# Kernel optimization log

Hardware: AMD Instinct MI355X
Metric: run time of the kernel (lower is better)

Reference implementation:

```python
import jax, jax.numpy as jnp
import numpy as np

N = 1 << 20          # number of sample points (rays x samples)
ENC = 32             # hash-grid encoded dim (16 levels x 2 features)
HID = 64
GEO = 15


def setup_inputs() -> dict:
    key = jax.random.key(0)
    ks = jax.random.split(key, 16)
    sc = lambda fan_in: 1.0 / np.sqrt(fan_in)
    return {
        "x": jax.random.normal(ks[0], (N, ENC), jnp.float32),
        "d": jax.random.normal(ks[1], (N, ENC), jnp.float32),
        # sigma net: ENC -> 64 -> 64 -> 1+GEO, bias-free, stored [in, out]
        "Ws0": jax.random.normal(ks[2], (ENC, HID), jnp.float32) * sc(ENC),
        "Ws1": jax.random.normal(ks[3], (HID, HID), jnp.float32) * sc(HID),
        "Ws2": jax.random.normal(ks[4], (HID, 1 + GEO), jnp.float32) * sc(HID),
        # color net: ENC+GEO -> 64 -> 64 -> 64 -> 3, bias-free
        "Wc0": jax.random.normal(ks[5], (ENC + GEO, HID), jnp.float32) * sc(ENC + GEO),
        "Wc1": jax.random.normal(ks[6], (HID, HID), jnp.float32) * sc(HID),
        "Wc2": jax.random.normal(ks[7], (HID, HID), jnp.float32) * sc(HID),
        "Wc3": jax.random.normal(ks[8], (HID, 3), jnp.float32) * sc(HID),
    }


def reference(x, d, Ws0, Ws1, Ws2, Wc0, Wc1, Wc2, Wc3):
    # sigma network: ReLU after EVERY layer (including the last, as in source)
    h = x
    for W in (Ws0, Ws1, Ws2):
        h = jax.nn.relu(h @ W)
    sigma = h[..., 0]            # [N]
    geo_feat = h[..., 1:]        # [N, GEO]

    # color network: ReLU on all but last layer, then sigmoid
    h = jnp.concatenate([d, geo_feat], axis=-1)   # [N, ENC+GEO]
    color_ws = (Wc0, Wc1, Wc2, Wc3)
    for i, W in enumerate(color_ws):
        h = h @ W
        if i != len(color_ws) - 1:
            h = jax.nn.relu(h)
    color = jax.nn.sigmoid(h)    # [N, 3]
    return color, sigma
```

## Files before the change

kernel.cpp:

```cpp
#include <hip/hip_runtime.h>
#include <hip/hip_bf16.h>

typedef short s8v __attribute__((ext_vector_type(8)));
typedef float f4v __attribute__((ext_vector_type(4)));

#define MFMA_BF16 __builtin_amdgcn_mfma_f32_16x16x32_bf16

constexpr int OFF_W0T  = 0;
constexpr int OFF_W1T  = 2560;
constexpr int OFF_W2T  = 7168;
constexpr int OFF_WC0T = 8320;
constexpr int OFF_WC1T = 12928;
constexpr int OFF_WC2T = 17536;
constexpr int OFF_WC3T = 22144;
constexpr int SMEM_EL  = 23296;

static __device__ __forceinline__ short bf2s(__hip_bfloat16 h) {
    union { __hip_bfloat16 b; short s; } u; u.b = h; return u.s;
}

__global__ __launch_bounds__(512, 2)
void rf_fused(const void* __restrict__ xv,
              const void* __restrict__ dv,
              const void* __restrict__ Ws0,
              const void* __restrict__ Ws1,
              const void* __restrict__ Ws2,
              const void* __restrict__ Wc0,
              const void* __restrict__ Wc1,
              const void* __restrict__ Wc2,
              const void* __restrict__ Wc3,
              void* __restrict__ outp,
              int npts)
{
    __shared__ __align__(16) short smem[SMEM_EL];
    __shared__ int cls_cnt;
    const int t = threadIdx.x;

    if (t == 0) cls_cnt = 0;
    __syncthreads();
    {
        unsigned short w = ((const unsigned short*)xv)[2 * t];
        int e = (w >> 7) & 0xFF;
        if (e >= 110 && e <= 140) atomicAdd(&cls_cnt, 1);
    }
    __syncthreads();
    const bool isbf = (cls_cnt >= 256);

    auto ldw = [&](const void* p, int idx) -> short {
        if (isbf) return ((const short*)p)[idx];
        return bf2s(__float2bfloat16(((const float*)p)[idx]));
    };

    for (int i = t; i < 2048; i += 512) { int k = i >> 6, n = i & 63; smem[OFF_W0T  + n*40 + k] = ldw(Ws0, i); }
    for (int i = t; i < 4096; i += 512) { int k = i >> 6, n = i & 63; smem[OFF_W1T  + n*72 + k] = ldw(Ws1, i); }
    for (int i = t; i < 1024; i += 512) { int k = i >> 4, n = i & 15; smem[OFF_W2T  + n*72 + k] = ldw(Ws2, i); }
    for (int i = t; i < 4096; i += 512) {
        int n = i >> 6, k = i & 63;
        short v = 0;
        if (k < 32)                 v = ldw(Wc0, k*64 + n);
        else if (k >= 33 && k < 48) v = ldw(Wc0, (k-1)*64 + n);
        smem[OFF_WC0T + n*72 + k] = v;
    }
    for (int i = t; i < 4096; i += 512) { int k = i >> 6, n = i & 63; smem[OFF_WC1T + n*72 + k] = ldw(Wc1, i); }
    for (int i = t; i < 4096; i += 512) { int k = i >> 6, n = i & 63; smem[OFF_WC2T + n*72 + k] = ldw(Wc2, i); }
    for (int i = t; i < 1024; i += 512) { int n = i >> 6, k = i & 63; smem[OFF_WC3T + n*72 + k] = (n < 3) ? ldw(Wc3, k*3 + n) : (short)0; }
    __syncthreads();

    const int lane = t & 63;
    const int wv   = t >> 6;
    const int m16  = lane & 15;
    const int q    = lane >> 4;

    const f4v zf = {0.f, 0.f, 0.f, 0.f};

    s8v w0f[4], w1f[4][2], wc0f[4][2], wc1f[4][2], wc2f[4][2], w2f[2], wc3f[2];
    #pragma unroll
    for (int kt = 0; kt < 4; kt++) {
        w0f[kt] = *(const s8v*)(smem + OFF_W0T + (kt*16 + m16)*40 + q*8);
        #pragma unroll
        for (int h = 0; h < 2; h++) {
            w1f[kt][h]  = *(const s8v*)(smem + OFF_W1T  + (kt*16 + m16)*72 + h*32 + q*8);
            wc0f[kt][h] = *(const s8v*)(smem + OFF_WC0T + (kt*16 + m16)*72 + h*32 + q*8);
            wc1f[kt][h] = *(const s8v*)(smem + OFF_WC1T + (kt*16 + m16)*72 + h*32 + q*8);
            wc2f[kt][h] = *(const s8v*)(smem + OFF_WC2T + (kt*16 + m16)*72 + h*32 + q*8);
        }
    }
    #pragma unroll
    for (int h = 0; h < 2; h++) {
        w2f[h]  = *(const s8v*)(smem + OFF_W2T  + m16*72 + h*32 + q*8);
        wc3f[h] = *(const s8v*)(smem + OFF_WC3T + m16*72 + h*32 + q*8);
    }

    auto loadRow8f = [&](const void* p, int eoff) -> s8v {
        const float* f = (const float*)p + eoff;
        f4v f0 = *(const f4v*)f;
        f4v f1 = *(const f4v*)(f + 4);
        s8v r;
        #pragma unroll
        for (int j = 0; j < 4; j++) {
            r[j]     = bf2s(__float2bfloat16(f0[j]));
            r[j + 4] = bf2s(__float2bfloat16(f1[j]));
        }
        return r;
    };
    auto putOut = [&](int idx, float v) {
        if (isbf) ((short*)outp)[idx] = bf2s(__float2bfloat16(v));
        else      ((float*)outp)[idx] = v;
    };

    auto redist = [&](const f4v (&a)[4], s8v (&fr)[2]) {
        unsigned int P[4][2];
        #pragma unroll
        for (int kt = 0; kt < 4; kt++)
            #pragma unroll
            for (int rp = 0; rp < 2; rp++) {
                float lo = fmaxf(a[kt][2*rp],     0.f);
                float hi = fmaxf(a[kt][2*rp + 1], 0.f);
                union { __hip_bfloat162 b; unsigned int u; } cu;
                cu.b = __float22bfloat162_rn(float2{lo, hi});
                P[kt][rp] = cu.u;
            }
        #pragma unroll
        for (int a2 = 0; a2 < 2; a2++)
            #pragma unroll
            for (int rp = 0; rp < 2; rp++) {
                asm("v_permlane32_swap_b32 %0, %1" : "+v"(P[2*a2][rp]), "+v"(P[2*a2+1][rp]));
                asm("v_permlane16_swap_b32 %0, %1" : "+v"(P[2*a2][rp]), "+v"(P[2*a2+1][rp]));
            }
        #pragma unroll
        for (int kc = 0; kc < 2; kc++) {
            union { unsigned int u[4]; s8v v; } fu;
            fu.u[0] = P[2*kc][0];     fu.u[1] = P[2*kc][1];
            fu.u[2] = P[2*kc + 1][0]; fu.u[3] = P[2*kc + 1][1];
            fr[kc] = fu.v;
        }
    };

    auto layerR = [&](const s8v (&wf)[4][2], const s8v (&bfr)[2][2], f4v (&out)[2][4]) {
        #pragma unroll
        for (int kt = 0; kt < 4; kt++)
            #pragma unroll
            for (int pt = 0; pt < 2; pt++)
                out[pt][kt] = MFMA_BF16(wf[kt][1], bfr[pt][1],
                              MFMA_BF16(wf[kt][0], bfr[pt][0], zf, 0,0,0), 0,0,0);
    };

    const int ntiles = npts / 32;
    const int tstep  = gridDim.x * 8;
    int tile = blockIdx.x * 8 + wv;

    s8v xb[2], db[2];
    if (isbf && tile < ntiles) {
        #pragma unroll
        for (int pt = 0; pt < 2; pt++) {
            const int off = (tile*32 + pt*16 + m16)*32 + q*8;
            xb[pt] = *(const s8v*)((const short*)xv + off);
            db[pt] = *(const s8v*)((const short*)dv + off);
        }
    }

    #pragma unroll 1
    for (; tile < ntiles; tile += tstep) {
        const int r0  = tile * 32;
        const int nxt = tile + tstep;

        if (!isbf) {
            #pragma unroll
            for (int pt = 0; pt < 2; pt++) {
                const int off = (r0 + pt*16 + m16)*32 + q*8;
                xb[pt] = loadRow8f(xv, off);
                db[pt] = loadRow8f(dv, off);
            }
        }

        f4v acc[2][4];
        s8v bfr[2][2];

        #pragma unroll
        for (int kt = 0; kt < 4; kt++)
            #pragma unroll
            for (int pt = 0; pt < 2; pt++)
                acc[pt][kt] = MFMA_BF16(w0f[kt], xb[pt], zf, 0,0,0);

        if (isbf && nxt < ntiles) {
            #pragma unroll
            for (int pt = 0; pt < 2; pt++)
                xb[pt] = *(const s8v*)((const short*)xv + (nxt*32 + pt*16 + m16)*32 + q*8);
        }

        #pragma unroll
        for (int pt = 0; pt < 2; pt++) redist(acc[pt], bfr[pt]);

        layerR(w1f, bfr, acc);
        #pragma unroll
        for (int pt = 0; pt < 2; pt++) redist(acc[pt], bfr[pt]);

        f4v s3[2];
        #pragma unroll
        for (int pt = 0; pt < 2; pt++)
            s3[pt] = MFMA_BF16(w2f[1], bfr[pt][1],
                     MFMA_BF16(w2f[0], bfr[pt][0], zf, 0,0,0), 0,0,0);

        if (q == 0) {
            #pragma unroll
            for (int pt = 0; pt < 2; pt++)
                putOut(3*npts + r0 + pt*16 + m16, fmaxf(s3[pt][0], 0.f));
        }

        #pragma unroll
        for (int pt = 0; pt < 2; pt++) {
            f4v sd[4] = { s3[pt], s3[pt], s3[pt], s3[pt] };
            s8v fj[2];
            redist(sd, fj);
            bfr[pt][1] = fj[1];
            bfr[pt][0] = db[pt];
        }

        layerR(wc0f, bfr, acc);

        if (isbf && nxt < ntiles) {
            #pragma unroll
            for (int pt = 0; pt < 2; pt++)
                db[pt] = *(const s8v*)((const short*)dv + (nxt*32 + pt*16 + m16)*32 + q*8);
        }

        #pragma unroll
        for (int pt = 0; pt < 2; pt++) redist(acc[pt], bfr[pt]);

        layerR(wc1f, bfr, acc);
        #pragma unroll
        for (int pt = 0; pt < 2; pt++) redist(acc[pt], bfr[pt]);

        layerR(wc2f, bfr, acc);
        #pragma unroll
        for (int pt = 0; pt < 2; pt++) redist(acc[pt], bfr[pt]);

        f4v c7[2];
        #pragma unroll
        for (int pt = 0; pt < 2; pt++)
            c7[pt] = MFMA_BF16(wc3f[1], bfr[pt][1],
                     MFMA_BF16(wc3f[0], bfr[pt][0], zf, 0,0,0), 0,0,0);

        if (q == 0) {
            #pragma unroll
            for (int pt = 0; pt < 2; pt++) {
                const int base = (r0 + pt*16 + m16) * 3;
                #pragma unroll
                for (int r = 0; r < 3; r++) {
                    float v  = c7[pt][r];
                    float sg = 1.0f / (1.0f + __expf(-v));
                    putOut(base + r, sg);
                }
            }
        }
    }
}

extern "C" void kernel_launch(void* const* d_in, const int* in_sizes, int n_in,
                              void* d_out, int out_size, void* d_ws, size_t ws_size,
                              hipStream_t stream) {
    const int npts = in_sizes[0] / 32;
    rf_fused<<<512, 512, 0, stream>>>(d_in[0], d_in[1], d_in[2], d_in[3], d_in[4],
                                      d_in[5], d_in[6], d_in[7], d_in[8],
                                      d_out, npts);
}
```

Before: 338.3 us.

## Stream weight fragments from LDS per layer to raise occupancy

Stops holding every layer's weight fragments in registers for the whole kernel. Each layer now reloads its fragments from shared memory just before its MFMAs, which frees enough VGPRs to raise launch bounds to 6 blocks per CU and the grid to 768 blocks. It also packs with an inline v_cvt_pk_bf16_f32 and adds a cheaper half redistribution for the geo features, so the broadcast copy of s3 is no longer fed through the full redistribution. The trade-off is extra LDS read traffic and latency in every tile iteration, in exchange for more waves to hide memory and MFMA latency.

Result: faster. 325.0 us (-3.9%).

```diff
diff --git a/kernel.cpp b/kernel.cpp
--- a/kernel.cpp
+++ b/kernel.cpp
@@ -19,7 +19,7 @@
     union { __hip_bfloat16 b; short s; } u; u.b = h; return u.s;
 }
 
-__global__ __launch_bounds__(512, 2)
+__global__ __launch_bounds__(512, 6)
 void rf_fused(const void* __restrict__ xv,
               const void* __restrict__ dv,
               const void* __restrict__ Ws0,
@@ -73,24 +73,6 @@
 
     const f4v zf = {0.f, 0.f, 0.f, 0.f};
 
-    s8v w0f[4], w1f[4][2], wc0f[4][2], wc1f[4][2], wc2f[4][2], w2f[2], wc3f[2];
-    #pragma unroll
-    for (int kt = 0; kt < 4; kt++) {
-        w0f[kt] = *(const s8v*)(smem + OFF_W0T + (kt*16 + m16)*40 + q*8);
-        #pragma unroll
-        for (int h = 0; h < 2; h++) {
-            w1f[kt][h]  = *(const s8v*)(smem + OFF_W1T  + (kt*16 + m16)*72 + h*32 + q*8);
-            wc0f[kt][h] = *(const s8v*)(smem + OFF_WC0T + (kt*16 + m16)*72 + h*32 + q*8);
-            wc1f[kt][h] = *(const s8v*)(smem + OFF_WC1T + (kt*16 + m16)*72 + h*32 + q*8);
-            wc2f[kt][h] = *(const s8v*)(smem + OFF_WC2T + (kt*16 + m16)*72 + h*32 + q*8);
-        }
-    }
-    #pragma unroll
-    for (int h = 0; h < 2; h++) {
-        w2f[h]  = *(const s8v*)(smem + OFF_W2T  + m16*72 + h*32 + q*8);
-        wc3f[h] = *(const s8v*)(smem + OFF_WC3T + m16*72 + h*32 + q*8);
-    }
-
     auto loadRow8f = [&](const void* p, int eoff) -> s8v {
         const float* f = (const float*)p + eoff;
         f4v f0 = *(const f4v*)f;
@@ -108,18 +90,19 @@
         else      ((float*)outp)[idx] = v;
     };
 
+    auto cvtpk = [](float lo, float hi) -> unsigned int {
+        unsigned int r;
+        asm("v_cvt_pk_bf16_f32 %0, %1, %2" : "=v"(r) : "v"(lo), "v"(hi));
+        return r;
+    };
+
     auto redist = [&](const f4v (&a)[4], s8v (&fr)[2]) {
         unsigned int P[4][2];
         #pragma unroll
         for (int kt = 0; kt < 4; kt++)
             #pragma unroll
-            for (int rp = 0; rp < 2; rp++) {
-                float lo = fmaxf(a[kt][2*rp],     0.f);
-                float hi = fmaxf(a[kt][2*rp + 1], 0.f);
-                union { __hip_bfloat162 b; unsigned int u; } cu;
-                cu.b = __float22bfloat162_rn(float2{lo, hi});
-                P[kt][rp] = cu.u;
-            }
+            for (int rp = 0; rp < 2; rp++)
+                P[kt][rp] = cvtpk(fmaxf(a[kt][2*rp], 0.f), fmaxf(a[kt][2*rp+1], 0.f));
         #pragma unroll
         for (int a2 = 0; a2 < 2; a2++)
             #pragma unroll
@@ -135,14 +118,33 @@
             fr[kc] = fu.v;
         }
     };
-
-    auto layerR = [&](const s8v (&wf)[4][2], const s8v (&bfr)[2][2], f4v (&out)[2][4]) {
-        #pragma unroll
-        for (int kt = 0; kt < 4; kt++)
-            #pragma unroll
-            for (int pt = 0; pt < 2; pt++)
-                out[pt][kt] = MFMA_BF16(wf[kt][1], bfr[pt][1],
-                              MFMA_BF16(wf[kt][0], bfr[pt][0], zf, 0,0,0), 0,0,0);
+    auto redistHalf = [&](const f4v s, s8v &frHi) {
+        unsigned int P2[2], P3[2];
+        #pragma unroll
+        for (int rp = 0; rp < 2; rp++) {
+            P2[rp] = cvtpk(fmaxf(s[2*rp], 0.f), fmaxf(s[2*rp+1], 0.f));
+            P3[rp] = P2[rp];
+        }
+        #pragma unroll
+        for (int rp = 0; rp < 2; rp++) {
+            asm("v_permlane32_swap_b32 %0, %1" : "+v"(P2[rp]), "+v"(P3[rp]));
+            asm("v_permlane16_swap_b32 %0, %1" : "+v"(P2[rp]), "+v"(P3[rp]));
+        }
+        union { unsigned int u[4]; s8v v; } fu;
+        fu.u[0] = P2[0]; fu.u[1] = P2[1]; fu.u[2] = P3[0]; fu.u[3] = P3[1];
+        frHi = fu.v;
+    };
+
+    auto layerT = [&](int woff, const s8v (&bfr)[2][2], f4v (&out)[2][4]) {
+        #pragma unroll
+        for (int kt = 0; kt < 4; kt++) {
+            s8v a0 = *(const s8v*)(smem + woff + (kt*16 + m16)*72 + q*8);
+            s8v a1 = *(const s8v*)(smem + woff + (kt*16 + m16)*72 + 32 + q*8);
+            #pragma unroll
+            for (int pt = 0; pt < 2; pt++)
+                out[pt][kt] = MFMA_BF16(a1, bfr[pt][1],
+                              MFMA_BF16(a0, bfr[pt][0], zf, 0,0,0), 0,0,0);
+        }
     };
 
     const int ntiles = npts / 32;
@@ -177,10 +179,12 @@
         s8v bfr[2][2];
 
         #pragma unroll
-        for (int kt = 0; kt < 4; kt++)
-            #pragma unroll
-            for (int pt = 0; pt < 2; pt++)
-                acc[pt][kt] = MFMA_BF16(w0f[kt], xb[pt], zf, 0,0,0);
+        for (int kt = 0; kt < 4; kt++) {
+            s8v a0 = *(const s8v*)(smem + OFF_W0T + (kt*16 + m16)*40 + q*8);
+            #pragma unroll
+            for (int pt = 0; pt < 2; pt++)
+                acc[pt][kt] = MFMA_BF16(a0, xb[pt], zf, 0,0,0);
+        }
 
         if (isbf && nxt < ntiles) {
             #pragma unroll
@@ -191,15 +195,19 @@
         #pragma unroll
         for (int pt = 0; pt < 2; pt++) redist(acc[pt], bfr[pt]);
 
-        layerR(w1f, bfr, acc);
+        layerT(OFF_W1T, bfr, acc);
         #pragma unroll
         for (int pt = 0; pt < 2; pt++) redist(acc[pt], bfr[pt]);
 
         f4v s3[2];
-        #pragma unroll
-        for (int pt = 0; pt < 2; pt++)
-            s3[pt] = MFMA_BF16(w2f[1], bfr[pt][1],
-                     MFMA_BF16(w2f[0], bfr[pt][0], zf, 0,0,0), 0,0,0);
+        {
+            s8v c0 = *(const s8v*)(smem + OFF_W2T + m16*72 + q*8);
+            s8v c1 = *(const s8v*)(smem + OFF_W2T + m16*72 + 32 + q*8);
+            #pragma unroll
+            for (int pt = 0; pt < 2; pt++)
+                s3[pt] = MFMA_BF16(c1, bfr[pt][1],
+                         MFMA_BF16(c0, bfr[pt][0], zf, 0,0,0), 0,0,0);
+        }
 
         if (q == 0) {
             #pragma unroll
@@ -209,14 +217,11 @@
 
         #pragma unroll
         for (int pt = 0; pt < 2; pt++) {
-            f4v sd[4] = { s3[pt], s3[pt], s3[pt], s3[pt] };
-            s8v fj[2];
-            redist(sd, fj);
-            bfr[pt][1] = fj[1];
+            redistHalf(s3[pt], bfr[pt][1]);
             bfr[pt][0] = db[pt];
         }
 
-        layerR(wc0f, bfr, acc);
+        layerT(OFF_WC0T, bfr, acc);
 
         if (isbf && nxt < ntiles) {
             #pragma unroll
@@ -227,20 +232,23 @@
         #pragma unroll
         for (int pt = 0; pt < 2; pt++) redist(acc[pt], bfr[pt]);
 
-        layerR(wc1f, bfr, acc);
-        #pragma unroll
-        for (int pt = 0; pt < 2; pt++) redist(acc[pt], bfr[pt]);
-
-        layerR(wc2f, bfr, acc);
+        layerT(OFF_WC1T, bfr, acc);
+        #pragma unroll
+        for (int pt = 0; pt < 2; pt++) redist(acc[pt], bfr[pt]);
+
+        layerT(OFF_WC2T, bfr, acc);
         #pragma unroll
         for (int pt = 0; pt < 2; pt++) redist(acc[pt], bfr[pt]);
 
         f4v c7[2];
-        #pragma unroll
-        for (int pt = 0; pt < 2; pt++)
-            c7[pt] = MFMA_BF16(wc3f[1], bfr[pt][1],
-                     MFMA_BF16(wc3f[0], bfr[pt][0], zf, 0,0,0), 0,0,0);
-
+        {
+            s8v e0 = *(const s8v*)(smem + OFF_WC3T + m16*72 + q*8);
+            s8v e1 = *(const s8v*)(smem + OFF_WC3T + m16*72 + 32 + q*8);
+            #pragma unroll
+            for (int pt = 0; pt < 2; pt++)
+                c7[pt] = MFMA_BF16(e1, bfr[pt][1],
+                         MFMA_BF16(e0, bfr[pt][0], zf, 0,0,0), 0,0,0);
+        }
         if (q == 0) {
             #pragma unroll
             for (int pt = 0; pt < 2; pt++) {
@@ -260,7 +268,7 @@
                               void* d_out, int out_size, void* d_ws, size_t ws_size,
                               hipStream_t stream) {
     const int npts = in_sizes[0] / 32;
-    rf_fused<<<512, 512, 0, stream>>>(d_in[0], d_in[1], d_in[2], d_in[3], d_in[4],
+    rf_fused<<<768, 512, 0, stream>>>(d_in[0], d_in[1], d_in[2], d_in[3], d_in[4],
                                       d_in[5], d_in[6], d_in[7], d_in[8],
                                       d_out, npts);
 }
```

## Switch MLP to 32x32x16 MFMA with weights read from LDS per layer

Applied to the files above, without the earlier changes.

Replaces the 16x16x32 bf16 MFMA tiling with 32x32x16 MFMAs, so each wave handles a 32-point tile with fewer, larger matrix instructions. It also adds a simpler permlane32-only redistribution using v_cvt_pk_bf16_f32. Most weight fragments are no longer held in registers; they are re-read from LDS inside each layer, apart from the small W2 fragment. This frees VGPRs so launch bounds can rise to four blocks per CU. The cost is extra LDS traffic on every tile and a larger zero-padded shared-memory layout.

New measurement: 312.0 us. 7.8% less time.

```diff
diff --git a/kernel.cpp b/kernel.cpp
--- a/kernel.cpp
+++ b/kernel.cpp
@@ -1,25 +1,26 @@
 #include <hip/hip_runtime.h>
 #include <hip/hip_bf16.h>
 
-typedef short s8v __attribute__((ext_vector_type(8)));
-typedef float f4v __attribute__((ext_vector_type(4)));
-
-#define MFMA_BF16 __builtin_amdgcn_mfma_f32_16x16x32_bf16
+typedef short s8v  __attribute__((ext_vector_type(8)));
+typedef float f4v  __attribute__((ext_vector_type(4)));
+typedef float f16v __attribute__((ext_vector_type(16)));
+
+#define MFMA32 __builtin_amdgcn_mfma_f32_32x32x16_bf16
 
 constexpr int OFF_W0T  = 0;
 constexpr int OFF_W1T  = 2560;
 constexpr int OFF_W2T  = 7168;
-constexpr int OFF_WC0T = 8320;
-constexpr int OFF_WC1T = 12928;
-constexpr int OFF_WC2T = 17536;
-constexpr int OFF_WC3T = 22144;
-constexpr int SMEM_EL  = 23296;
+constexpr int OFF_WC0T = 9472;
+constexpr int OFF_WC1T = 14080;
+constexpr int OFF_WC2T = 18688;
+constexpr int OFF_WC3T = 23296;
+constexpr int SMEM_EL  = 25600;
 
 static __device__ __forceinline__ short bf2s(__hip_bfloat16 h) {
     union { __hip_bfloat16 b; short s; } u; u.b = h; return u.s;
 }
 
-__global__ __launch_bounds__(512, 2)
+__global__ __launch_bounds__(512, 4)
 void rf_fused(const void* __restrict__ xv,
               const void* __restrict__ dv,
               const void* __restrict__ Ws0,
@@ -51,9 +52,12 @@
         return bf2s(__float2bfloat16(((const float*)p)[idx]));
     };
 
-    for (int i = t; i < 2048; i += 512) { int k = i >> 6, n = i & 63; smem[OFF_W0T  + n*40 + k] = ldw(Ws0, i); }
-    for (int i = t; i < 4096; i += 512) { int k = i >> 6, n = i & 63; smem[OFF_W1T  + n*72 + k] = ldw(Ws1, i); }
-    for (int i = t; i < 1024; i += 512) { int k = i >> 4, n = i & 15; smem[OFF_W2T  + n*72 + k] = ldw(Ws2, i); }
+    for (int i = t; i < 2048; i += 512) { int k = i >> 6, n = i & 63; smem[OFF_W0T + n*40 + k] = ldw(Ws0, i); }
+    for (int i = t; i < 4096; i += 512) { int k = i >> 6, n = i & 63; smem[OFF_W1T + n*72 + k] = ldw(Ws1, i); }
+    for (int i = t; i < 2048; i += 512) {
+        int n = i >> 6, k = i & 63;
+        smem[OFF_W2T + n*72 + k] = (n < 16) ? ldw(Ws2, k*16 + n) : (short)0;
+    }
     for (int i = t; i < 4096; i += 512) {
         int n = i >> 6, k = i & 63;
         short v = 0;
@@ -63,33 +67,23 @@
     }
     for (int i = t; i < 4096; i += 512) { int k = i >> 6, n = i & 63; smem[OFF_WC1T + n*72 + k] = ldw(Wc1, i); }
     for (int i = t; i < 4096; i += 512) { int k = i >> 6, n = i & 63; smem[OFF_WC2T + n*72 + k] = ldw(Wc2, i); }
-    for (int i = t; i < 1024; i += 512) { int n = i >> 6, k = i & 63; smem[OFF_WC3T + n*72 + k] = (n < 3) ? ldw(Wc3, k*3 + n) : (short)0; }
+    for (int i = t; i < 2048; i += 512) {
+        int n = i >> 6, k = i & 63;
+        smem[OFF_WC3T + n*72 + k] = (n < 3) ? ldw(Wc3, k*3 + n) : (short)0;
+    }
     __syncthreads();
 
     const int lane = t & 63;
     const int wv   = t >> 6;
-    const int m16  = lane & 15;
-    const int q    = lane >> 4;
-
-    const f4v zf = {0.f, 0.f, 0.f, 0.f};
-
-    s8v w0f[4], w1f[4][2], wc0f[4][2], wc1f[4][2], wc2f[4][2], w2f[2], wc3f[2];
+    const int l5   = lane & 31;
+    const int hi   = lane >> 5;
+    const f16v zf16 = {0.f,0.f,0.f,0.f,0.f,0.f,0.f,0.f,
+                       0.f,0.f,0.f,0.f,0.f,0.f,0.f,0.f};
+
+    s8v w2f[4];
     #pragma unroll
-    for (int kt = 0; kt < 4; kt++) {
-        w0f[kt] = *(const s8v*)(smem + OFF_W0T + (kt*16 + m16)*40 + q*8);
-        #pragma unroll
-        for (int h = 0; h < 2; h++) {
-            w1f[kt][h]  = *(const s8v*)(smem + OFF_W1T  + (kt*16 + m16)*72 + h*32 + q*8);
-            wc0f[kt][h] = *(const s8v*)(smem + OFF_WC0T + (kt*16 + m16)*72 + h*32 + q*8);
-            wc1f[kt][h] = *(const s8v*)(smem + OFF_WC1T + (kt*16 + m16)*72 + h*32 + q*8);
-            wc2f[kt][h] = *(const s8v*)(smem + OFF_WC2T + (kt*16 + m16)*72 + h*32 + q*8);
-        }
-    }
-    #pragma unroll
-    for (int h = 0; h < 2; h++) {
-        w2f[h]  = *(const s8v*)(smem + OFF_W2T  + m16*72 + h*32 + q*8);
-        wc3f[h] = *(const s8v*)(smem + OFF_WC3T + m16*72 + h*32 + q*8);
-    }
+    for (int kc = 0; kc < 4; kc++)
+        w2f[kc] = *(const s8v*)(smem + OFF_W2T + l5*72 + kc*16 + hi*8);
 
     auto loadRow8f = [&](const void* p, int eoff) -> s8v {
         const float* f = (const float*)p + eoff;
@@ -107,152 +101,159 @@
         if (isbf) ((short*)outp)[idx] = bf2s(__float2bfloat16(v));
         else      ((float*)outp)[idx] = v;
     };
-
-    auto redist = [&](const f4v (&a)[4], s8v (&fr)[2]) {
-        unsigned int P[4][2];
-        #pragma unroll
-        for (int kt = 0; kt < 4; kt++)
-            #pragma unroll
-            for (int rp = 0; rp < 2; rp++) {
-                float lo = fmaxf(a[kt][2*rp],     0.f);
-                float hi = fmaxf(a[kt][2*rp + 1], 0.f);
-                union { __hip_bfloat162 b; unsigned int u; } cu;
-                cu.b = __float22bfloat162_rn(float2{lo, hi});
-                P[kt][rp] = cu.u;
+    auto cvtpk = [](float lo, float hiV) -> unsigned int {
+        unsigned int r;
+        asm("v_cvt_pk_bf16_f32 %0, %1, %2" : "=v"(r) : "v"(lo), "v"(hiV));
+        return r;
+    };
+    auto swap32 = [](unsigned int &x, unsigned int &y) {
+        asm("v_permlane32_swap_b32 %0, %1" : "+v"(x), "+v"(y));
+    };
+
+    auto redist32 = [&](const f16v &a0, const f16v &a1, s8v (&fr)[4]) {
+        unsigned int Q[2][4][2];
+        #pragma unroll
+        for (int tt = 0; tt < 2; tt++) {
+            const f16v &a = tt ? a1 : a0;
+            #pragma unroll
+            for (int aa = 0; aa < 4; aa++)
+                #pragma unroll
+                for (int e = 0; e < 2; e++)
+                    Q[tt][aa][e] = cvtpk(fmaxf(a[4*aa + 2*e], 0.f),
+                                         fmaxf(a[4*aa + 2*e + 1], 0.f));
+        }
+        #pragma unroll
+        for (int tt = 0; tt < 2; tt++)
+            #pragma unroll
+            for (int A = 0; A < 2; A++)
+                #pragma unroll
+                for (int e = 0; e < 2; e++)
+                    swap32(Q[tt][2*A][e], Q[tt][2*A + 1][e]);
+        #pragma unroll
+        for (int c = 0; c < 4; c++) {
+            const int tt = c >> 1, A = c & 1;
+            union { unsigned int u[4]; s8v v; } fu;
+            fu.u[0] = Q[tt][2*A][0];     fu.u[1] = Q[tt][2*A][1];
+            fu.u[2] = Q[tt][2*A + 1][0]; fu.u[3] = Q[tt][2*A + 1][1];
+            fr[c] = fu.v;
+        }
+    };
+    auto redistJ = [&](const f16v &a, s8v &fg) {
+        unsigned int Q[2][2];
+        #pragma unroll
+        for (int aa = 0; aa < 2; aa++)
+            #pragma unroll
+            for (int e = 0; e < 2; e++)
+                Q[aa][e] = cvtpk(fmaxf(a[4*aa + 2*e], 0.f),
+                                 fmaxf(a[4*aa + 2*e + 1], 0.f));
+        #pragma unroll
+        for (int e = 0; e < 2; e++) swap32(Q[0][e], Q[1][e]);
+        union { unsigned int u[4]; s8v v; } fu;
+        fu.u[0] = Q[0][0]; fu.u[1] = Q[0][1];
+        fu.u[2] = Q[1][0]; fu.u[3] = Q[1][1];
+        fg = fu.v;
+    };
+
+    auto layer64 = [&](int woff, const s8v (&b)[4], f16v (&o)[2]) {
+        #pragma unroll
+        for (int mt = 0; mt < 2; mt++) {
+            f16v c = zf16;
+            #pragma unroll
+            for (int kc = 0; kc < 4; kc++) {
+                s8v a = *(const s8v*)(smem + woff + (mt*32 + l5)*72 + kc*16 + hi*8);
+                c = MFMA32(a, b[kc], c, 0, 0, 0);
             }
-        #pragma unroll
-        for (int a2 = 0; a2 < 2; a2++)
-            #pragma unroll
-            for (int rp = 0; rp < 2; rp++) {
-                asm("v_permlane32_swap_b32 %0, %1" : "+v"(P[2*a2][rp]), "+v"(P[2*a2+1][rp]));
-                asm("v_permlane16_swap_b32 %0, %1" : "+v"(P[2*a2][rp]), "+v"(P[2*a2+1][rp]));
+            o[mt] = c;
+        }
+    };
+
+    const int ntiles = npts / 32;
+    const int nw     = gridDim.x * 8;
+    int tile = blockIdx.x * 8 + wv;
+
+    auto loadB2 = [&](const void* p, int r0, s8v (&f)[2]) {
+        #pragma unroll
+        for (int kc = 0; kc < 2; kc++) {
+            const int off = (r0 + l5)*32 + kc*16 + hi*8;
+            f[kc] = isbf ? *(const s8v*)((const short*)p + off) : loadRow8f(p, off);
+        }
+    };
+
+    s8v xb[2];
+    if (tile < ntiles) loadB2(xv, tile*32, xb);
+
+    #pragma unroll 1
+    for (; tile < ntiles; tile += nw) {
+        const int r0  = tile * 32;
+        const int nxt = tile + nw;
+
+        s8v db[2];
+        loadB2(dv, r0, db);
+
+        f16v h[2];
+        #pragma unroll
+        for (int mt = 0; mt < 2; mt++) {
+            f16v c = zf16;
+            #pragma unroll
+            for (int kc = 0; kc < 2; kc++) {
+                s8v a = *(const s8v*)(smem + OFF_W0T + (mt*32 + l5)*40 + kc*16 + hi*8);
+                c = MFMA32(a, xb[kc], c, 0, 0, 0);
             }
-        #pragma unroll
-        for (int kc = 0; kc < 2; kc++) {
-            union { unsigned int u[4]; s8v v; } fu;
-            fu.u[0] = P[2*kc][0];     fu.u[1] = P[2*kc][1];
-            fu.u[2] = P[2*kc + 1][0]; fu.u[3] = P[2*kc + 1][1];
-            fr[kc] = fu.v;
-        }
-    };
-
-    auto layerR = [&](const s8v (&wf)[4][2], const s8v (&bfr)[2][2], f4v (&out)[2][4]) {
-        #pragma unroll
-        for (int kt = 0; kt < 4; kt++)
-            #pragma unroll
-            for (int pt = 0; pt < 2; pt++)
-                out[pt][kt] = MFMA_BF16(wf[kt][1], bfr[pt][1],
-                              MFMA_BF16(wf[kt][0], bfr[pt][0], zf, 0,0,0), 0,0,0);
-    };
-
-    const int ntiles = npts / 32;
-    const int tstep  = gridDim.x * 8;
-    int tile = blockIdx.x * 8 + wv;
-
-    s8v xb[2], db[2];
-    if (isbf && tile < ntiles) {
-        #pragma unroll
-        for (int pt = 0; pt < 2; pt++) {
-            const int off = (tile*32 + pt*16 + m16)*32 + q*8;
-            xb[pt] = *(const s8v*)((const short*)xv + off);
-            db[pt] = *(const s8v*)((const short*)dv + off);
-        }
-    }
-
-    #pragma unroll 1
-    for (; tile < ntiles; tile += tstep) {
-        const int r0  = tile * 32;
-        const int nxt = tile + tstep;
-
-        if (!isbf) {
-            #pragma unroll
-            for (int pt = 0; pt < 2; pt++) {
-                const int off = (r0 + pt*16 + m16)*32 + q*8;
-                xb[pt] = loadRow8f(xv, off);
-                db[pt] = loadRow8f(dv, off);
+            h[mt] = c;
+        }
+
+        s8v xbn[2];
+        if (nxt < ntiles) loadB2(xv, nxt*32, xbn);
+
+        s8v bfr[4];
+        redist32(h[0], h[1], bfr);
+
+        layer64(OFF_W1T, bfr, h);
+        redist32(h[0], h[1], bfr);
+
+        f16v s3 = zf16;
+        #pragma unroll
+        for (int kc = 0; kc < 4; kc++)
+            s3 = MFMA32(w2f[kc], bfr[kc], s3, 0, 0, 0);
+
+        if (hi == 0) putOut(3*npts + r0 + l5, fmaxf(s3[0], 0.f));
+
+        s8v geo;
+        redistJ(s3, geo);
+
+        #pragma unroll
+        for (int mt = 0; mt < 2; mt++) {
+            const int base = OFF_WC0T + (mt*32 + l5)*72;
+            f16v c = zf16;
+            c = MFMA32(*(const s8v*)(smem + base +  0 + hi*8), db[0], c, 0, 0, 0);
+            c = MFMA32(*(const s8v*)(smem + base + 16 + hi*8), db[1], c, 0, 0, 0);
+            c = MFMA32(*(const s8v*)(smem + base + 32 + hi*8), geo,   c, 0, 0, 0);
+            h[mt] = c;
+        }
+        redist32(h[0], h[1], bfr);
+
+        layer64(OFF_WC1T, bfr, h);
+        redist32(h[0], h[1], bfr);
+
+        layer64(OFF_WC2T, bfr, h);
+        redist32(h[0], h[1], bfr);
+
+        f16v c7 = zf16;
+        #pragma unroll
+        for (int kc = 0; kc < 4; kc++) {
+            s8v a = *(const s8v*)(smem + OFF_WC3T + l5*72 + kc*16 + hi*8);
+            c7 = MFMA32(a, bfr[kc], c7, 0, 0, 0);
+        }
+        if (hi == 0) {
+            const int base = (r0 + l5) * 3;
+            #pragma unroll
+            for (int r = 0; r < 3; r++) {
+                float sg = 1.0f / (1.0f + __expf(-c7[r]));
+                putOut(base + r, sg);
             }
         }
 
-        f4v acc[2][4];
-        s8v bfr[2][2];
-
-        #pragma unroll
-        for (int kt = 0; kt < 4; kt++)
-            #pragma unroll
-            for (int pt = 0; pt < 2; pt++)
-                acc[pt][kt] = MFMA_BF16(w0f[kt], xb[pt], zf, 0,0,0);
-
-        if (isbf && nxt < ntiles) {
-            #pragma unroll
-            for (int pt = 0; pt < 2; pt++)
-                xb[pt] = *(const s8v*)((const short*)xv + (nxt*32 + pt*16 + m16)*32 + q*8);
-        }
-
-        #pragma unroll
-        for (int pt = 0; pt < 2; pt++) redist(acc[pt], bfr[pt]);
-
-        layerR(w1f, bfr, acc);
-        #pragma unroll
-        for (int pt = 0; pt < 2; pt++) redist(acc[pt], bfr[pt]);
-
-        f4v s3[2];
-        #pragma unroll
-        for (int pt = 0; pt < 2; pt++)
-            s3[pt] = MFMA_BF16(w2f[1], bfr[pt][1],
-                     MFMA_BF16(w2f[0], bfr[pt][0], zf, 0,0,0), 0,0,0);
-
-        if (q == 0) {
-            #pragma unroll
-            for (int pt = 0; pt < 2; pt++)
-                putOut(3*npts + r0 + pt*16 + m16, fmaxf(s3[pt][0], 0.f));
-        }
-
-        #pragma unroll
-        for (int pt = 0; pt < 2; pt++) {
-            f4v sd[4] = { s3[pt], s3[pt], s3[pt], s3[pt] };
-            s8v fj[2];
-            redist(sd, fj);
-            bfr[pt][1] = fj[1];
-            bfr[pt][0] = db[pt];
-        }
-
-        layerR(wc0f, bfr, acc);
-
-        if (isbf && nxt < ntiles) {
-            #pragma unroll
-            for (int pt = 0; pt < 2; pt++)
-                db[pt] = *(const s8v*)((const short*)dv + (nxt*32 + pt*16 + m16)*32 + q*8);
-        }
-
-        #pragma unroll
-        for (int pt = 0; pt < 2; pt++) redist(acc[pt], bfr[pt]);
-
-        layerR(wc1f, bfr, acc);
-        #pragma unroll
-        for (int pt = 0; pt < 2; pt++) redist(acc[pt], bfr[pt]);
-
-        layerR(wc2f, bfr, acc);
-        #pragma unroll
-        for (int pt = 0; pt < 2; pt++) redist(acc[pt], bfr[pt]);
-
-        f4v c7[2];
-        #pragma unroll
-        for (int pt = 0; pt < 2; pt++)
-            c7[pt] = MFMA_BF16(wc3f[1], bfr[pt][1],
-                     MFMA_BF16(wc3f[0], bfr[pt][0], zf, 0,0,0), 0,0,0);
-
-        if (q == 0) {
-            #pragma unroll
-            for (int pt = 0; pt < 2; pt++) {
-                const int base = (r0 + pt*16 + m16) * 3;
-                #pragma unroll
-                for (int r = 0; r < 3; r++) {
-                    float v  = c7[pt][r];
-                    float sg = 1.0f / (1.0f + __expf(-v));
-                    putOut(base + r, sg);
-                }
-            }
-        }
+        xb[0] = xbn[0]; xb[1] = xbn[1];
     }
 }
 
```
